# Optimization experiments

Hardware: AMD Instinct MI355X
Metric: run time of the kernel (lower is better)

## Reference

```python
import jax, jax.numpy as jnp
import numpy as np

L, T, B, I, H = 2, 512, 32, 512, 512


def setup_inputs() -> dict:
    key = jax.random.key(0)
    ks = jax.random.split(key, 3)
    # xavier-uniform-ish scale for weights
    def xav(k, shape, fan_in, fan_out):
        lim = float(np.sqrt(6.0 / (fan_in + fan_out)))
        return jax.random.uniform(k, shape, jnp.float32, -lim, lim)
    x = jax.random.normal(ks[0], (T, B, I), jnp.float32)
    w_ih = xav(ks[1], (L, 4 * H, I), I, 4 * H)
    w_hh = xav(ks[2], (L, 4 * H, H), H, 4 * H)
    b_ih = jnp.zeros((L, 4 * H), jnp.float32)
    b_hh = jnp.zeros((L, 4 * H), jnp.float32)
    return {"x": x, "w_ih": w_ih, "w_hh": w_hh, "b_ih": b_ih, "b_hh": b_hh}


def _run_layer(x, Wih, Whh, bih, bhh):
    # x: [T, B, in]; precompute all input-hidden projections as one GEMM
    pre = jnp.einsum('tbi,gi->tbg', x, Wih) + bih + bhh  # [T, B, 4H]
    hdim = Whh.shape[1]
    h0 = jnp.zeros((x.shape[1], hdim), x.dtype)
    c0 = jnp.zeros((x.shape[1], hdim), x.dtype)

    def step(carry, pre_t):
        h, c = carry
        gates = pre_t + h @ Whh.T  # [B, 4H]
        i_t = jax.nn.sigmoid(gates[:, 0 * hdim:1 * hdim])
        f_t = jax.nn.sigmoid(gates[:, 1 * hdim:2 * hdim])
        g_t = jnp.tanh(gates[:, 2 * hdim:3 * hdim])
        o_t = jax.nn.sigmoid(gates[:, 3 * hdim:4 * hdim])
        c_new = f_t * c + i_t * g_t
        h_new = o_t * jnp.tanh(c_new)
        return (h_new, c_new), (h_new, c_new, i_t, f_t, g_t, o_t)

    _, outs = jax.lax.scan(step, (h0, c0), pre)
    return outs  # each [T, B, H]


def reference(x, w_ih, w_hh, b_ih, b_hh):
    num_layers = w_ih.shape[0]
    all_outs = []
    layer_in = x
    for l in range(num_layers):
        outs = _run_layer(layer_in, w_ih[l], w_hh[l], b_ih[l], b_hh[l])
        all_outs.append(outs)
        layer_in = outs[0]  # h of this layer feeds next
    # stack per-quantity across layers -> each [L, T, B, H]
    stacked = tuple(jnp.stack([all_outs[l][q] for l in range(num_layers)], axis=0)
                    for q in range(6))
    return stacked  # (h, c, i, f, g, o)
```

## Files before the change

kernel.cpp:

```cpp
#include <hip/hip_runtime.h>
#include <cstdint>
#include <cstddef>

#define TT   512
#define BB   32
#define HH   512
#define KK   512
#define QS   16777216
#define LTBH 8388608
#define NBLK 16

typedef __attribute__((ext_vector_type(8))) __bf16 bf16x8;
typedef __attribute__((ext_vector_type(8))) short  s16x8;
typedef __attribute__((ext_vector_type(4))) short  s16x4;
typedef __attribute__((ext_vector_type(4))) float  f32x4;

#define MFMA(a, b, c) c = __builtin_amdgcn_mfma_f32_16x16x32_bf16(a, b, c, 0, 0, 0)

static __device__ __forceinline__ unsigned short f2bf_rne(float f) {
  unsigned u = __float_as_uint(f);
  u += 0x7fffu + ((u >> 16) & 1u);
  return (unsigned short)(u >> 16);
}

static __device__ __forceinline__ bf16x8 load_f32_bf8(const float* __restrict__ p) {
  uint4 a = *(const uint4*)p;
  uint4 b = *(const uint4*)(p + 4);
  s16x8 r;
  r[0] = (short)(a.x >> 16); r[1] = (short)(a.y >> 16);
  r[2] = (short)(a.z >> 16); r[3] = (short)(a.w >> 16);
  r[4] = (short)(b.x >> 16); r[5] = (short)(b.y >> 16);
  r[6] = (short)(b.z >> 16); r[7] = (short)(b.w >> 16);
  return __builtin_bit_cast(bf16x8, r);
}

static __device__ __forceinline__ bf16x8 load_bf8(const short* __restrict__ p) {
  return __builtin_bit_cast(bf16x8, *(const s16x8*)p);
}

static __device__ __forceinline__ float fsig(float x) {
  return __builtin_amdgcn_rcpf(1.0f + __expf(-x));
}
static __device__ __forceinline__ float ftanh(float x) {
  return 2.0f * __builtin_amdgcn_rcpf(1.0f + __expf(-2.0f * x)) - 1.0f;
}

__global__ void zero_kernel(int* __restrict__ p, int n) {
  int i = blockIdx.x * 256 + threadIdx.x;
  if (i < n) p[i] = 0;
}

__global__ void wconv_kernel(const float* __restrict__ s, short* __restrict__ d, int n4) {
  int i = blockIdx.x * 256 + threadIdx.x;
  if (i < n4) {
    uint4 v = ((const uint4*)s)[i];
    s16x4 o;
    o[0] = (short)f2bf_rne(__uint_as_float(v.x));
    o[1] = (short)f2bf_rne(__uint_as_float(v.y));
    o[2] = (short)f2bf_rne(__uint_as_float(v.z));
    o[3] = (short)f2bf_rne(__uint_as_float(v.w));
    ((s16x4*)d)[i] = o;
  }
}

__global__ __launch_bounds__(256, 1) void lstm_scan_all(
    const float* __restrict__ x,
    const short* __restrict__ wihb,
    const short* __restrict__ whhb,
    const float* __restrict__ bihg,
    const float* __restrict__ bhhg,
    float* __restrict__ out,
    short* __restrict__ hbuf,
    int* __restrict__ cnt)
{
  __shared__ float gsm[4][32][33];
  __shared__ float csm[32][33];
  __shared__ float biasm[4][32];

  const int layer = blockIdx.x >> 4;
  const int w     = blockIdx.x & 15;
  const int j0    = w * 32;
  const int tid   = threadIdx.x;
  const int wave  = tid >> 6;
  const int lane  = tid & 63;
  const int l16   = lane & 15;
  const int kg    = lane >> 4;
  const int koff  = kg * 8;

  const float* __restrict__ xin = layer ? out : x;
  const short* __restrict__ wih = wihb + (size_t)layer * (4 * HH * KK);
  const short* __restrict__ whh = whhb + (size_t)layer * (4 * HH * KK);
  float* __restrict__ outb = out + (size_t)layer * LTBH;
  short* __restrict__ hb   = hbuf + layer * (2 * BB * HH);
  int* __restrict__ mycnt  = cnt + layer;
  int* __restrict__ cnt0   = cnt;

  for (int idx = tid; idx < 32 * 33; idx += 256) (&csm[0][0])[idx] = 0.0f;
  if (tid < 128) {
    int q = tid >> 5, jj = tid & 31;
    biasm[q][jj] = bihg[layer * 2048 + q * 512 + j0 + jj]
                 + bhhg[layer * 2048 + q * 512 + j0 + jj];
  }
  __syncthreads();

  const int gb = wave * 512 + j0;
  const short* __restrict__ wi0 = wih + (size_t)(gb      + l16) * KK + koff;
  const short* __restrict__ wi1 = wih + (size_t)(gb + 16 + l16) * KK + koff;
  const short* __restrict__ wh0 = whh + (size_t)(gb      + l16) * KK + koff;
  const short* __restrict__ wh1 = whh + (size_t)(gb + 16 + l16) * KK + koff;

  const int actb = tid >> 3;
  const int actj = (tid & 7) * 4;

  for (int t = 0; t < TT; ++t) {
    if (layer == 1) {
      if (tid == 0) {
        const int tgt = (t + 1) * NBLK;
        while (__hip_atomic_load(cnt0, __ATOMIC_ACQUIRE, __HIP_MEMORY_SCOPE_AGENT) < tgt)
          __builtin_amdgcn_s_sleep(1);
      }
      __syncthreads();
    }

    f32x4 a00 = {0.f, 0.f, 0.f, 0.f}, a01 = a00, a10 = a00, a11 = a00;

    const float* __restrict__ xr0 = xin + (size_t)t * (BB * KK) + (size_t)l16 * KK + koff;
    const float* __restrict__ xr1 = xr0 + 16 * KK;
    const short* __restrict__ hr0 = hb + (t & 1) * (BB * HH) + l16 * HH + koff;
    const short* __restrict__ hr1 = hr0 + 16 * HH;

#pragma unroll 4
    for (int kc = 0; kc < KK; kc += 32) {
      bf16x8 fa0 = load_f32_bf8(xr0 + kc);
      bf16x8 fa1 = load_f32_bf8(xr1 + kc);
      bf16x8 fb0 = load_bf8(wi0 + kc);
      bf16x8 fb1 = load_bf8(wi1 + kc);
      MFMA(fa0, fb0, a00); MFMA(fa0, fb1, a01);
      MFMA(fa1, fb0, a10); MFMA(fa1, fb1, a11);
    }
#pragma unroll 4
    for (int kc = 0; kc < HH; kc += 32) {
      bf16x8 fa0 = load_bf8(hr0 + kc);
      bf16x8 fa1 = load_bf8(hr1 + kc);
      bf16x8 fb0 = load_bf8(wh0 + kc);
      bf16x8 fb1 = load_bf8(wh1 + kc);
      MFMA(fa0, fb0, a00); MFMA(fa0, fb1, a01);
      MFMA(fa1, fb0, a10); MFMA(fa1, fb1, a11);
    }

    const int r0 = kg * 4;
#pragma unroll
    for (int r = 0; r < 4; ++r) {
      gsm[wave][r0 + r][l16]           = a00[r];
      gsm[wave][r0 + r][16 + l16]      = a01[r];
      gsm[wave][16 + r0 + r][l16]      = a10[r];
      gsm[wave][16 + r0 + r][16 + l16] = a11[r];
    }
    __syncthreads();

    {
      f32x4 vh, vc, vi, vf, vg, vo;
      s16x4 hnext;
#pragma unroll
      for (int u = 0; u < 4; ++u) {
        const int jj = actj + u;
        float gi = gsm[0][actb][jj] + biasm[0][jj];
        float gf = gsm[1][actb][jj] + biasm[1][jj];
        float gg = gsm[2][actb][jj] + biasm[2][jj];
        float go = gsm[3][actb][jj] + biasm[3][jj];
        float iv = fsig(gi), fv = fsig(gf), gv = ftanh(gg), ov = fsig(go);
        float cv = fv * csm[actb][jj] + iv * gv;
        csm[actb][jj] = cv;
        float hv = ov * ftanh(cv);
        vh[u] = hv; vc[u] = cv; vi[u] = iv; vf[u] = fv; vg[u] = gv; vo[u] = ov;
        hnext[u] = (short)f2bf_rne(hv);
      }
      float* __restrict__ po = outb + (size_t)t * (BB * HH) + (size_t)actb * HH + j0 + actj;
      *(f32x4*)(po)               = vh;
      *(f32x4*)(po + (size_t)QS)      = vc;
      *(f32x4*)(po + (size_t)2 * QS)  = vi;
      *(f32x4*)(po + (size_t)3 * QS)  = vf;
      *(f32x4*)(po + (size_t)4 * QS)  = vg;
      *(f32x4*)(po + (size_t)5 * QS)  = vo;
      *(s16x4*)(hb + ((t + 1) & 1) * (BB * HH) + actb * HH + j0 + actj) = hnext;
    }

    __threadfence();
    __syncthreads();
    if (tid == 0) {
      __hip_atomic_fetch_add(mycnt, 1, __ATOMIC_RELEASE, __HIP_MEMORY_SCOPE_AGENT);
      if (t + 1 < TT) {
        const int tgt = (t + 1) * NBLK;
        while (__hip_atomic_load(mycnt, __ATOMIC_ACQUIRE, __HIP_MEMORY_SCOPE_AGENT) < tgt)
          __builtin_amdgcn_s_sleep(1);
      }
    }
    __syncthreads();
  }
}

extern "C" void kernel_launch(void* const* d_in, const int* in_sizes, int n_in,
                              void* d_out, int out_size, void* d_ws, size_t ws_size,
                              hipStream_t stream) {
  const float* x    = (const float*)d_in[0];
  const float* w_ih = (const float*)d_in[1];
  const float* w_hh = (const float*)d_in[2];
  const float* b_ih = (const float*)d_in[3];
  const float* b_hh = (const float*)d_in[4];
  float* out = (float*)d_out;

  short* wihb = (short*)d_ws;
  short* whhb = wihb + 2097152;
  short* hbuf = whhb + 2097152;
  int*   cnt  = (int*)(hbuf + 65536);

  zero_kernel<<<(32770 + 255) / 256, 256, 0, stream>>>((int*)hbuf, 32768 + 2);
  wconv_kernel<<<2048, 256, 0, stream>>>(w_ih, wihb, 524288);
  wconv_kernel<<<2048, 256, 0, stream>>>(w_hh, whhb, 524288);
  lstm_scan_all<<<32, 256, 0, stream>>>(x, wihb, whhb, b_ih, b_hh, out, hbuf, cnt);
}
```

Before: 17.40 ms.

## Replace fenced barrier with 4-deep bf16 h ring and relaxed atomic handoff

Layer outputs h are now passed through a 4-slot bf16 ring buffer per layer, written with relaxed agent-scope atomic stores and read with agent-scope atomic loads. Layer 1 takes its input from layer 0's ring instead of re-reading fp32 output from global memory. Layer 0 is throttled by a counter from layer 1 so slots are not overwritten too early. The heavy __threadfence and the end-of-step spin are replaced by an s_waitcnt, a relaxed counter increment and a spin at the start of the next step, shortening the critical path per timestep. Relying on relaxed ordering plus waitcnt for cross-block visibility carries a memory-ordering risk.

```diff
diff --git a/kernel.cpp b/kernel.cpp
--- a/kernel.cpp
+++ b/kernel.cpp
@@ -9,11 +9,13 @@
 #define QS   16777216
 #define LTBH 8388608
 #define NBLK 16
+#define RING 65536
 
 typedef __attribute__((ext_vector_type(8))) __bf16 bf16x8;
 typedef __attribute__((ext_vector_type(8))) short  s16x8;
 typedef __attribute__((ext_vector_type(4))) short  s16x4;
 typedef __attribute__((ext_vector_type(4))) float  f32x4;
+typedef __attribute__((ext_vector_type(2))) unsigned long long u64x2;
 
 #define MFMA(a, b, c) c = __builtin_amdgcn_mfma_f32_16x16x32_bf16(a, b, c, 0, 0, 0)
 
@@ -36,6 +38,20 @@
 
 static __device__ __forceinline__ bf16x8 load_bf8(const short* __restrict__ p) {
   return __builtin_bit_cast(bf16x8, *(const s16x8*)p);
+}
+
+static __device__ __forceinline__ bf16x8 load_bf8_agent(const short* p) {
+  u64x2 v;
+  v[0] = __hip_atomic_load((const unsigned long long*)p,
+                           __ATOMIC_RELAXED, __HIP_MEMORY_SCOPE_AGENT);
+  v[1] = __hip_atomic_load((const unsigned long long*)(p + 4),
+                           __ATOMIC_RELAXED, __HIP_MEMORY_SCOPE_AGENT);
+  return __builtin_bit_cast(bf16x8, v);
+}
+
+static __device__ __forceinline__ void spin_ge(int* p, int tgt) {
+  while (__hip_atomic_load(p, __ATOMIC_RELAXED, __HIP_MEMORY_SCOPE_AGENT) < tgt)
+    __builtin_amdgcn_s_sleep(1);
 }
 
 static __device__ __forceinline__ float fsig(float x) {
@@ -70,7 +86,7 @@
     const float* __restrict__ bihg,
     const float* __restrict__ bhhg,
     float* __restrict__ out,
-    short* __restrict__ hbuf,
+    short* __restrict__ hring,
     int* __restrict__ cnt)
 {
   __shared__ float gsm[4][32][33];
@@ -87,13 +103,14 @@
   const int kg    = lane >> 4;
   const int koff  = kg * 8;
 
-  const float* __restrict__ xin = layer ? out : x;
   const short* __restrict__ wih = wihb + (size_t)layer * (4 * HH * KK);
   const short* __restrict__ whh = whhb + (size_t)layer * (4 * HH * KK);
   float* __restrict__ outb = out + (size_t)layer * LTBH;
-  short* __restrict__ hb   = hbuf + layer * (2 * BB * HH);
-  int* __restrict__ mycnt  = cnt + layer;
+  short* __restrict__ ring0  = hring;
+  short* __restrict__ myring = hring + layer * RING;
+  int* __restrict__ mycnt  = cnt + layer * 32;
   int* __restrict__ cnt0   = cnt;
+  int* __restrict__ cnt1   = cnt + 32;
 
   for (int idx = tid; idx < 32 * 33; idx += 256) (&csm[0][0])[idx] = 0.0f;
   if (tid < 128) {
@@ -113,39 +130,56 @@
   const int actj = (tid & 7) * 4;
 
   for (int t = 0; t < TT; ++t) {
-    if (layer == 1) {
-      if (tid == 0) {
-        const int tgt = (t + 1) * NBLK;
-        while (__hip_atomic_load(cnt0, __ATOMIC_ACQUIRE, __HIP_MEMORY_SCOPE_AGENT) < tgt)
-          __builtin_amdgcn_s_sleep(1);
-      }
-      __syncthreads();
-    }
+    if (tid == 0) {
+      if (layer == 1) {
+        spin_ge(cnt0, (t + 1) * NBLK);
+      } else if (t >= 4) {
+        spin_ge(cnt1, (t - 3) * NBLK);
+      }
+      if (t) spin_ge(mycnt, t * NBLK);
+    }
+    __syncthreads();
 
     f32x4 a00 = {0.f, 0.f, 0.f, 0.f}, a01 = a00, a10 = a00, a11 = a00;
 
-    const float* __restrict__ xr0 = xin + (size_t)t * (BB * KK) + (size_t)l16 * KK + koff;
-    const float* __restrict__ xr1 = xr0 + 16 * KK;
-    const short* __restrict__ hr0 = hb + (t & 1) * (BB * HH) + l16 * HH + koff;
-    const short* __restrict__ hr1 = hr0 + 16 * HH;
-
+    if (layer == 0) {
+      const float* __restrict__ xr0 = x + (size_t)t * (BB * KK) + (size_t)l16 * KK + koff;
+      const float* __restrict__ xr1 = xr0 + 16 * KK;
 #pragma unroll 4
-    for (int kc = 0; kc < KK; kc += 32) {
-      bf16x8 fa0 = load_f32_bf8(xr0 + kc);
-      bf16x8 fa1 = load_f32_bf8(xr1 + kc);
-      bf16x8 fb0 = load_bf8(wi0 + kc);
-      bf16x8 fb1 = load_bf8(wi1 + kc);
-      MFMA(fa0, fb0, a00); MFMA(fa0, fb1, a01);
-      MFMA(fa1, fb0, a10); MFMA(fa1, fb1, a11);
-    }
+      for (int kc = 0; kc < KK; kc += 32) {
+        bf16x8 fa0 = load_f32_bf8(xr0 + kc);
+        bf16x8 fa1 = load_f32_bf8(xr1 + kc);
+        bf16x8 fb0 = load_bf8(wi0 + kc);
+        bf16x8 fb1 = load_bf8(wi1 + kc);
+        MFMA(fa0, fb0, a00); MFMA(fa0, fb1, a01);
+        MFMA(fa1, fb0, a10); MFMA(fa1, fb1, a11);
+      }
+    } else {
+      const short* xr0 = ring0 + ((t + 1) & 3) * (BB * HH) + l16 * HH + koff;
+      const short* xr1 = xr0 + 16 * HH;
 #pragma unroll 4
-    for (int kc = 0; kc < HH; kc += 32) {
-      bf16x8 fa0 = load_bf8(hr0 + kc);
-      bf16x8 fa1 = load_bf8(hr1 + kc);
-      bf16x8 fb0 = load_bf8(wh0 + kc);
-      bf16x8 fb1 = load_bf8(wh1 + kc);
-      MFMA(fa0, fb0, a00); MFMA(fa0, fb1, a01);
-      MFMA(fa1, fb0, a10); MFMA(fa1, fb1, a11);
+      for (int kc = 0; kc < KK; kc += 32) {
+        bf16x8 fa0 = load_bf8_agent(xr0 + kc);
+        bf16x8 fa1 = load_bf8_agent(xr1 + kc);
+        bf16x8 fb0 = load_bf8(wi0 + kc);
+        bf16x8 fb1 = load_bf8(wi1 + kc);
+        MFMA(fa0, fb0, a00); MFMA(fa0, fb1, a01);
+        MFMA(fa1, fb0, a10); MFMA(fa1, fb1, a11);
+      }
+    }
+
+    {
+      const short* hr0 = myring + (t & 3) * (BB * HH) + l16 * HH + koff;
+      const short* hr1 = hr0 + 16 * HH;
+#pragma unroll 4
+      for (int kc = 0; kc < HH; kc += 32) {
+        bf16x8 fa0 = load_bf8_agent(hr0 + kc);
+        bf16x8 fa1 = load_bf8_agent(hr1 + kc);
+        bf16x8 fb0 = load_bf8(wh0 + kc);
+        bf16x8 fb1 = load_bf8(wh1 + kc);
+        MFMA(fa0, fb0, a00); MFMA(fa0, fb1, a01);
+        MFMA(fa1, fb0, a10); MFMA(fa1, fb1, a11);
+      }
     }
 
     const int r0 = kg * 4;
@@ -182,20 +216,16 @@
       *(f32x4*)(po + (size_t)3 * QS)  = vf;
       *(f32x4*)(po + (size_t)4 * QS)  = vg;
       *(f32x4*)(po + (size_t)5 * QS)  = vo;
-      *(s16x4*)(hb + ((t + 1) & 1) * (BB * HH) + actb * HH + j0 + actj) = hnext;
-    }
-
-    __threadfence();
+      __hip_atomic_store(
+          (unsigned long long*)(myring + ((t + 1) & 3) * (BB * HH) + actb * HH + j0 + actj),
+          __builtin_bit_cast(unsigned long long, hnext),
+          __ATOMIC_RELAXED, __HIP_MEMORY_SCOPE_AGENT);
+    }
+
+    asm volatile("s_waitcnt vmcnt(0)" ::: "memory");
     __syncthreads();
-    if (tid == 0) {
-      __hip_atomic_fetch_add(mycnt, 1, __ATOMIC_RELEASE, __HIP_MEMORY_SCOPE_AGENT);
-      if (t + 1 < TT) {
-        const int tgt = (t + 1) * NBLK;
-        while (__hip_atomic_load(mycnt, __ATOMIC_ACQUIRE, __HIP_MEMORY_SCOPE_AGENT) < tgt)
-          __builtin_amdgcn_s_sleep(1);
-      }
-    }
-    __syncthreads();
+    if (tid == 0)
+      __hip_atomic_fetch_add(mycnt, 1, __ATOMIC_RELAXED, __HIP_MEMORY_SCOPE_AGENT);
   }
 }
 
@@ -209,13 +239,13 @@
   const float* b_hh = (const float*)d_in[4];
   float* out = (float*)d_out;
 
-  short* wihb = (short*)d_ws;
-  short* whhb = wihb + 2097152;
-  short* hbuf = whhb + 2097152;
-  int*   cnt  = (int*)(hbuf + 65536);
-
-  zero_kernel<<<(32770 + 255) / 256, 256, 0, stream>>>((int*)hbuf, 32768 + 2);
+  short* wihb  = (short*)d_ws;
+  short* whhb  = wihb + 2097152;
+  short* hring = whhb + 2097152;
+  int*   cnt   = (int*)(hring + 131072);
+
+  zero_kernel<<<(65600 + 255) / 256, 256, 0, stream>>>((int*)hring, 65536 + 64);
   wconv_kernel<<<2048, 256, 0, stream>>>(w_ih, wihb, 524288);
   wconv_kernel<<<2048, 256, 0, stream>>>(w_hh, whhb, 524288);
-  lstm_scan_all<<<32, 256, 0, stream>>>(x, wihb, whhb, b_ih, b_hh, out, hbuf, cnt);
-}
+  lstm_scan_all<<<32, 256, 0, stream>>>(x, wihb, whhb, b_ih, b_hh, out, hring, cnt);
+}
```

After: 17.37 ms. Within noise of the previous version (-0.2%).
